# Kernel optimization log

Hardware: AMD Instinct MI355X
Metric: run time of the kernel (lower is better)

## Reference

```python
import jax, jax.numpy as jnp
import numpy as np

B, F, DIM = 32, 2048, 1024
H, DH, Q, DEPTH, MULT = 16, 64, 64, 6, 2
INNER = H * DH  # 1024
EPS = 1e-5


def _ln(x, g, b):
    m = jnp.mean(x, axis=-1, keepdims=True)
    v = jnp.mean((x - m) ** 2, axis=-1, keepdims=True)
    return (x - m) / jnp.sqrt(v + EPS) * g + b


def setup_inputs() -> dict:
    key = jax.random.key(0)
    ks = iter(jax.random.split(key, 32))
    def rn(shape, s=0.02):
        return jax.random.normal(next(ks), shape, dtype=jnp.float32) * s
    inp = {
        "features": jax.random.normal(next(ks), (B, F, DIM), dtype=jnp.float32),
        "mask": jax.random.randint(next(ks), (B, F), 0, 2),
        "latents": jax.random.normal(next(ks), (Q, INNER), dtype=jnp.float32),
        "W_down": rn((DIM, INNER)),
        "nin_g": jnp.ones((DIM,)), "nin_b": jnp.zeros((DIM,)),
        "lf_g": jnp.ones((DEPTH, INNER)), "lf_b": jnp.zeros((DEPTH, INNER)),
        "ll_g": jnp.ones((DEPTH, INNER)), "ll_b": jnp.zeros((DEPTH, INNER)),
        "Wq": rn((DEPTH, INNER, INNER)),
        "Wk": rn((DEPTH, INNER, INNER)),
        "Wv": rn((DEPTH, INNER, INNER)),
        "ffln_g": jnp.ones((DEPTH, INNER)), "ffln_b": jnp.zeros((DEPTH, INNER)),
        "ff_w1": rn((DEPTH, INNER, MULT * INNER)),
        "ff_w2": rn((DEPTH, MULT * INNER, INNER)),
        "nout_g": jnp.ones((INNER,)), "nout_b": jnp.zeros((INNER,)),
    }
    return inp


def reference(features, mask, latents, W_down, nin_g, nin_b, lf_g, lf_b, ll_g, ll_b,
              Wq, Wk, Wv, ffln_g, ffln_b, ff_w1, ff_w2, nout_g, nout_b):
    scale = DH ** (-0.5)
    # input norm + projection down to inner_dim
    f = _ln(features, nin_g, nin_b) @ W_down            # (B, F, INNER)
    x = jnp.broadcast_to(latents, (B, Q, INNER))        # (B, Q, INNER)
    keep = (mask != 0)[:, None, None, :]                # (B, 1, 1, F)
    for i in range(DEPTH):
        xf = _ln(f, lf_g[i], lf_b[i])
        xl = _ln(x, ll_g[i], ll_b[i])
        q = (xl @ Wq[i]).reshape(B, Q, H, DH).transpose(0, 2, 1, 3) * scale  # bhqd
        k = (xf @ Wk[i]).reshape(B, F, H, DH).transpose(0, 2, 1, 3)          # bhfd
        v = (xf @ Wv[i]).reshape(B, F, H, DH).transpose(0, 2, 1, 3)          # bhfd
        sim = jnp.einsum('bhqd,bhfd->bhqf', q, k)
        sim = sim - jax.lax.stop_gradient(jnp.max(sim, axis=-1, keepdims=True))
        sim = jnp.where(keep, sim, -jnp.inf)
        alphas = jax.nn.softmax(sim, axis=-1)
        alphas = jnp.nan_to_num(alphas, nan=0.0)        # fully-masked rows -> 0
        out = jnp.einsum('bhqf,bhfd->bqhd', alphas, v).reshape(B, Q, INNER)
        # feed-forward: LN -> Linear -> ReLU -> Linear
        h = jax.nn.relu(_ln(out, ffln_g[i], ffln_b[i]) @ ff_w1[i]) @ ff_w2[i]
        x = x + h
    return _ln(x, nout_g, nout_b)
```

## Files before the change

kernel.cpp:

```cpp
#include <hip/hip_runtime.h>
#include <stdint.h>


#define DEV static __device__ __forceinline__

typedef __attribute__((ext_vector_type(8))) short short8;
typedef __attribute__((ext_vector_type(4))) float f32x4;
typedef __attribute__((ext_vector_type(4))) int int4v;
typedef __attribute__((ext_vector_type(4))) unsigned short ushort4v;
typedef unsigned short ushort_t;

DEV float bf2f(ushort_t u){ union{uint32_t i; float f;} x; x.i = ((uint32_t)u)<<16; return x.f; }
DEV ushort_t f2bf(float f){
  union{float f; uint32_t i;} x; x.f = f;
  uint32_t r = x.i + 0x7fffu + ((x.i>>16)&1u);
  return (ushort_t)(r>>16);
}

#define GLOAD16(gp, lp) __builtin_amdgcn_global_load_lds( \
    (const __attribute__((address_space(1))) uint32_t*)(gp), \
    (__attribute__((address_space(3))) uint32_t*)(lp), 16, 0, 0)

#define VMCNT(n) asm volatile("s_waitcnt vmcnt(" #n ")" ::: "memory")
#define CFENCE   asm volatile("" ::: "memory")
#define MFMA16(a,b,c) __builtin_amdgcn_mfma_f32_16x16x32_bf16(a,b,c,0,0,0)
#define MFMAI8(a,b,c) __builtin_amdgcn_mfma_i32_16x16x64_i8(a,b,c,0,0,0)

template<int NXB>
DEV void xcd_remapN(int g, int total, int& x, int& y){
  int xcd = g & 7;
  int k = g >> 3;
  int rows_per_xcd = (total / NXB) >> 3;
  y = xcd * rows_per_xcd + (k / NXB);
  x = k % NXB;
}

DEV void wreduce2(float& a, float& b){
  #pragma unroll
  for (int d = 32; d; d >>= 1){ a += __shfl_xor(a, d); b += __shfl_xor(b, d); }
}

__global__ __launch_bounds__(256) void k_compact(const int* __restrict__ mask,
                                                 int* __restrict__ idx, int* __restrict__ cnt){
  int b = blockIdx.x, t = threadIdx.x;
  const int* mb = mask + b*2048;
  int keep[8]; int c = 0;
  #pragma unroll
  for (int u = 0; u < 8; ++u){ keep[u] = (mb[t*8+u] != 0); c += keep[u]; }
  __shared__ int s[256];
  s[t] = c; __syncthreads();
  for (int off = 1; off < 256; off <<= 1){
    int v = (t >= off) ? s[t-off] : 0;
    __syncthreads();
    s[t] += v;
    __syncthreads();
  }
  int pos = s[t] - c;
  #pragma unroll
  for (int u = 0; u < 8; ++u) if (keep[u]) idx[b*2048 + pos++] = t*8 + u;
  if (t == 255) cnt[b] = s[255];
}

__global__ __launch_bounds__(256) void k_gather_norm(const float* __restrict__ feat,
        const int* __restrict__ idx, const int* __restrict__ cnt, ushort_t* __restrict__ outp){
  int w = threadIdx.x >> 6, l = threadIdx.x & 63;
  int row = blockIdx.x*4 + w;
  int b = row >> 11, j = row & 2047;
  if (j >= cnt[b]) return;
  int src = idx[b*2048 + j];
  const float* rp = feat + ((size_t)(b*2048 + src))*1024;
  float4 v[4]; float s = 0.f, q = 0.f;
  #pragma unroll
  for (int i = 0; i < 4; ++i){
    v[i] = *(const float4*)(rp + i*256 + l*4);
    s += v[i].x+v[i].y+v[i].z+v[i].w;
    q += v[i].x*v[i].x+v[i].y*v[i].y+v[i].z*v[i].z+v[i].w*v[i].w;
  }
  wreduce2(s, q);
  float mean = s * (1.f/1024.f);
  float rstd = rsqrtf(q*(1.f/1024.f) - mean*mean + 1e-5f);
  ushort_t* op = outp + (size_t)row*1024;
  #pragma unroll
  for (int i = 0; i < 4; ++i){
    ushort4v o;
    o.x = f2bf((v[i].x-mean)*rstd); o.y = f2bf((v[i].y-mean)*rstd);
    o.z = f2bf((v[i].z-mean)*rstd); o.w = f2bf((v[i].w-mean)*rstd);
    *(ushort4v*)(op + i*256 + l*4) = o;
  }
}

__global__ __launch_bounds__(256) void k_rownorm_bf16(const ushort_t* __restrict__ in,
        ushort_t* __restrict__ outp, const int* __restrict__ cnt){
  int w = threadIdx.x >> 6, l = threadIdx.x & 63;
  int row = blockIdx.x*4 + w;
  if (cnt){ int b = row >> 11; if ((row & 2047) >= cnt[b]) return; }
  const ushort_t* rp = in + (size_t)row*1024;
  float f[4][4]; float s = 0.f, q = 0.f;
  #pragma unroll
  for (int i = 0; i < 4; ++i){
    ushort4v u = *(const ushort4v*)(rp + i*256 + l*4);
    f[i][0] = bf2f(u.x); f[i][1] = bf2f(u.y); f[i][2] = bf2f(u.z); f[i][3] = bf2f(u.w);
    #pragma unroll
    for (int jj = 0; jj < 4; ++jj){ s += f[i][jj]; q += f[i][jj]*f[i][jj]; }
  }
  wreduce2(s, q);
  float mean = s * (1.f/1024.f);
  float rstd = rsqrtf(q*(1.f/1024.f) - mean*mean + 1e-5f);
  ushort_t* op = outp + (size_t)row*1024;
  #pragma unroll
  for (int i = 0; i < 4; ++i){
    ushort4v o;
    o.x = f2bf((f[i][0]-mean)*rstd); o.y = f2bf((f[i][1]-mean)*rstd);
    o.z = f2bf((f[i][2]-mean)*rstd); o.w = f2bf((f[i][3]-mean)*rstd);
    *(ushort4v*)(op + i*256 + l*4) = o;
  }
}

__global__ __launch_bounds__(256) void k_rownorm_i8(const ushort_t* __restrict__ in,
        int8_t* __restrict__ outp, float* __restrict__ sca, const int* __restrict__ cnt){
  int w = threadIdx.x >> 6, l = threadIdx.x & 63;
  int row = blockIdx.x*4 + w;
  int b = row >> 11; if ((row & 2047) >= cnt[b]) return;
  const ushort_t* rp = in + (size_t)row*1024 + l*16;
  float f[16]; float s = 0.f, q = 0.f;
  #pragma unroll
  for (int i = 0; i < 4; ++i){
    ushort4v u = *(const ushort4v*)(rp + i*4);
    f[i*4+0] = bf2f(u.x); f[i*4+1] = bf2f(u.y);
    f[i*4+2] = bf2f(u.z); f[i*4+3] = bf2f(u.w);
  }
  #pragma unroll
  for (int jj = 0; jj < 16; ++jj){ s += f[jj]; q += f[jj]*f[jj]; }
  wreduce2(s, q);
  float mean = s * (1.f/1024.f);
  float rstd = rsqrtf(q*(1.f/1024.f) - mean*mean + 1e-5f);
  float amax = 0.f;
  #pragma unroll
  for (int jj = 0; jj < 16; ++jj) amax = fmaxf(amax, fabsf(f[jj]-mean));
  #pragma unroll
  for (int d = 32; d; d >>= 1) amax = fmaxf(amax, __shfl_xor(amax, d));
  amax *= rstd;
  float inv = (amax > 0.f) ? 127.f/amax : 0.f;
  if (l == 0) sca[row] = amax * (1.f/127.f);
  uint32_t wds[4];
  #pragma unroll
  for (int i = 0; i < 4; ++i){
    uint32_t wd = 0;
    #pragma unroll
    for (int c = 0; c < 4; ++c){
      int qv = (int)rintf((f[i*4+c]-mean)*rstd*inv);
      wd |= ((uint32_t)(uint8_t)(int8_t)qv) << (c*8);
    }
    wds[i] = wd;
  }
  int4v pk; pk[0]=(int)wds[0]; pk[1]=(int)wds[1]; pk[2]=(int)wds[2]; pk[3]=(int)wds[3];
  *(int4v*)(outp + (size_t)row*1024 + l*16) = pk;
}

__global__ __launch_bounds__(256) void k_quantW(const ushort_t* __restrict__ in,
        int8_t* __restrict__ outp, float* __restrict__ sca){
  int w = threadIdx.x >> 6, l = threadIdx.x & 63;
  int row = blockIdx.x*4 + w;
  const ushort_t* rp = in + (size_t)row*1024 + l*16;
  float f[16];
  #pragma unroll
  for (int i = 0; i < 4; ++i){
    ushort4v u = *(const ushort4v*)(rp + i*4);
    f[i*4+0] = bf2f(u.x); f[i*4+1] = bf2f(u.y);
    f[i*4+2] = bf2f(u.z); f[i*4+3] = bf2f(u.w);
  }
  float amax = 0.f;
  #pragma unroll
  for (int jj = 0; jj < 16; ++jj) amax = fmaxf(amax, fabsf(f[jj]));
  #pragma unroll
  for (int d = 32; d; d >>= 1) amax = fmaxf(amax, __shfl_xor(amax, d));
  float inv = (amax > 0.f) ? 127.f/amax : 0.f;
  if (l == 0) sca[row] = amax * (1.f/127.f);
  uint32_t wds[4];
  #pragma unroll
  for (int i = 0; i < 4; ++i){
    uint32_t wd = 0;
    #pragma unroll
    for (int c = 0; c < 4; ++c){
      int qv = (int)rintf(f[i*4+c]*inv);
      wd |= ((uint32_t)(uint8_t)(int8_t)qv) << (c*8);
    }
    wds[i] = wd;
  }
  int4v pk; pk[0]=(int)wds[0]; pk[1]=(int)wds[1]; pk[2]=(int)wds[2]; pk[3]=(int)wds[3];
  *(int4v*)(outp + (size_t)row*1024 + l*16) = pk;
}

__global__ __launch_bounds__(256) void k_rownorm_f32(const float* __restrict__ in,
                                                     ushort_t* __restrict__ outp){
  int w = threadIdx.x >> 6, l = threadIdx.x & 63;
  int row = blockIdx.x*4 + w;
  const float* rp = in + (size_t)row*1024;
  float4 v[4]; float s = 0.f, q = 0.f;
  #pragma unroll
  for (int i = 0; i < 4; ++i){
    v[i] = *(const float4*)(rp + i*256 + l*4);
    s += v[i].x+v[i].y+v[i].z+v[i].w;
    q += v[i].x*v[i].x+v[i].y*v[i].y+v[i].z*v[i].z+v[i].w*v[i].w;
  }
  wreduce2(s, q);
  float mean = s * (1.f/1024.f);
  float rstd = rsqrtf(q*(1.f/1024.f) - mean*mean + 1e-5f);
  ushort_t* op = outp + (size_t)row*1024;
  #pragma unroll
  for (int i = 0; i < 4; ++i){
    ushort4v o;
    o.x = f2bf((v[i].x-mean)*rstd); o.y = f2bf((v[i].y-mean)*rstd);
    o.z = f2bf((v[i].z-mean)*rstd); o.w = f2bf((v[i].w-mean)*rstd);
    *(ushort4v*)(op + i*256 + l*4) = o;
  }
}

__global__ __launch_bounds__(256) void k_final_ln(const float* __restrict__ x,
        const float* __restrict__ g, const float* __restrict__ bb, float* __restrict__ outp){
  int w = threadIdx.x >> 6, l = threadIdx.x & 63;
  int row = blockIdx.x*4 + w;
  const float* rp = x + (size_t)row*1024;
  float4 v[4]; float s = 0.f, q = 0.f;
  #pragma unroll
  for (int i = 0; i < 4; ++i){
    v[i] = *(const float4*)(rp + i*256 + l*4);
    s += v[i].x+v[i].y+v[i].z+v[i].w;
    q += v[i].x*v[i].x+v[i].y*v[i].y+v[i].z*v[i].z+v[i].w*v[i].w;
  }
  wreduce2(s, q);
  float mean = s * (1.f/1024.f);
  float rstd = rsqrtf(q*(1.f/1024.f) - mean*mean + 1e-5f);
  float* op = outp + (size_t)row*1024;
  #pragma unroll
  for (int i = 0; i < 4; ++i){
    float4 gg = *(const float4*)(g + i*256 + l*4);
    float4 bv = *(const float4*)(bb + i*256 + l*4);
    float4 o;
    o.x = (v[i].x-mean)*rstd*gg.x + bv.x; o.y = (v[i].y-mean)*rstd*gg.y + bv.y;
    o.z = (v[i].z-mean)*rstd*gg.z + bv.z; o.w = (v[i].w-mean)*rstd*gg.w + bv.w;
    *(float4*)(op + i*256 + l*4) = o;
  }
}

__global__ __launch_bounds__(256) void k_init_x(const float* __restrict__ lat, float* __restrict__ x){
  int v = blockIdx.x*256 + threadIdx.x;
  int row = v >> 8, cv = v & 255;
  ((float4*)x)[v] = ((const float4*)lat)[(row & 63)*256 + cv];
}

DEV void foldT_body(const float* __restrict__ W, const float* __restrict__ g,
                    float scale, ushort_t* __restrict__ Wt, int K, int N,
                    int n0, int k0){
  __shared__ float Ts[64][65];
  int t = threadIdx.x;
  #pragma unroll
  for (int i = 0; i < 4; ++i){
    int flat = i*1024 + t*4; int r = flat >> 6, c = flat & 63;
    float4 v = *(const float4*)(W + (size_t)(k0+r)*N + n0 + c);
    float gg = (g ? g[k0+r] : 1.f) * scale;
    Ts[r][c] = v.x*gg; Ts[r][c+1] = v.y*gg; Ts[r][c+2] = v.z*gg; Ts[r][c+3] = v.w*gg;
  }
  __syncthreads();
  #pragma unroll
  for (int i = 0; i < 4; ++i){
    int flat = i*1024 + t*4; int rn = flat >> 6, ck = flat & 63;
    ushort4v o;
    o.x = f2bf(Ts[ck][rn]);   o.y = f2bf(Ts[ck+1][rn]);
    o.z = f2bf(Ts[ck+2][rn]); o.w = f2bf(Ts[ck+3][rn]);
    *(ushort4v*)(Wt + (size_t)(n0+rn)*K + k0 + ck) = o;
  }
}

struct FDesc { const float* W; const float* g; ushort_t* dst; float scale; int K; int N; };
#define MAXFD 32
struct FoldTArgs { int cnt; FDesc d[MAXFD]; };

__global__ __launch_bounds__(256) void k_foldT_all(FoldTArgs a){
  const FDesc d = a.d[blockIdx.y];
  int nxb = d.N >> 6;
  int n0 = (blockIdx.x % nxb) * 64;
  int k0 = (blockIdx.x / nxb) * 64;
  if (k0 >= d.K) return;
  foldT_body(d.W, d.g, d.scale, d.dst, d.K, d.N, n0, k0);
}

DEV void foldBias_body(const float* __restrict__ W, const float* __restrict__ bvec,
                       float scale, float* __restrict__ bias, int K, int N, int o0){
  int t = threadIdx.x;
  int ol = t & 31, kc = t >> 5;
  int o = o0 + ol;
  int chunk = K >> 3;
  int c0 = kc*chunk, c1 = c0 + chunk;
  float s0 = 0, s1 = 0, s2 = 0, s3 = 0;
  for (int c = c0; c < c1; c += 4){
    s0 += bvec[c+0]*W[(size_t)(c+0)*N + o];
    s1 += bvec[c+1]*W[(size_t)(c+1)*N + o];
    s2 += bvec[c+2]*W[(size_t)(c+2)*N + o];
    s3 += bvec[c+3]*W[(size_t)(c+3)*N + o];
  }
  __shared__ float red[8][32];
  red[kc][ol] = (s0+s1)+(s2+s3);
  __syncthreads();
  if (kc == 0){
    float tot = 0;
    #pragma unroll
    for (int jj = 0; jj < 8; ++jj) tot += red[jj][ol];
    bias[o] = tot * scale;
  }
}

struct BDesc { const float* W; const float* b; float* dst; float scale; int K; int N; };
#define MAXBD 25
struct BiasArgs { int cnt; BDesc d[MAXBD]; };

__global__ __launch_bounds__(256) void k_foldBias_all(BiasArgs a){
  const BDesc d = a.d[blockIdx.y];
  int o0 = blockIdx.x * 32;
  if (o0 >= d.N) return;
  foldBias_body(d.W, d.b, d.scale, d.dst, d.K, d.N, o0);
}

template<int OUTMODE, bool SKIP>
__global__ __launch_bounds__(256, 4) void k_gemm(const ushort_t* __restrict__ A,
        const ushort_t* __restrict__ Bt, const float* __restrict__ bias,
        void* __restrict__ Cp, int M, int N, int K, const int* __restrict__ cnt){
  const int n0 = blockIdx.x * 128;
  const int m0 = blockIdx.y * 128;
  if (SKIP){ int b = m0 >> 11; if ((m0 & 2047) >= cnt[b]) return; }
  __shared__ ushort_t sA[2][128*32];
  __shared__ ushort_t sB[2][128*32];
  const int tid = threadIdx.x;
  const int wave = tid >> 6, lane = tid & 63;
  const int lo = lane & 15, hi = lane >> 4;
  const int wr = wave >> 1, wc = wave & 1;

  auto stage = [&](int buf, int k0){
    #pragma unroll
    for (int p = 0; p < 2; ++p){
      int r = p*64 + wave*16 + (lane >> 2);
      int c = lane & 3;
      {
        const ushort_t* gp = A + (size_t)(m0 + r)*K + k0 + c*8;
        char* lp = (char*)(&sA[buf][0]) + p*4096 + wave*1024;
        GLOAD16(gp, lp);
      }
      {
        const ushort_t* gp = Bt + (size_t)(n0 + r)*K + k0 + c*8;
        char* lp = (char*)(&sB[buf][0]) + p*4096 + wave*1024;
        GLOAD16(gp, lp);
      }
    }
  };

  f32x4 acc[4][4] = {};
  stage(0, 0);
  const int nk = K >> 5;
  for (int ks = 0; ks < nk; ++ks){
    __syncthreads();
    if (ks + 1 < nk) stage((ks+1)&1, (ks+1) << 5);
    const int buf = ks & 1;
    short8 af[4], bfr[4];
    #pragma unroll
    for (int mi = 0; mi < 4; ++mi)
      af[mi] = *(const short8*)(&sA[buf][(wr*64 + mi*16 + lo)*32 + hi*8]);
    #pragma unroll
    for (int ni = 0; ni < 4; ++ni)
      bfr[ni] = *(const short8*)(&sB[buf][(wc*64 + ni*16 + lo)*32 + hi*8]);
    #pragma unroll
    for (int mi = 0; mi < 4; ++mi)
      #pragma unroll
      for (int ni = 0; ni < 4; ++ni)
        acc[mi][ni] = MFMA16(af[mi], bfr[ni], acc[mi][ni]);
  }
  #pragma unroll
  for (int ni = 0; ni < 4; ++ni){
    int col = n0 + wc*64 + ni*16 + lo;
    float bv = bias ? bias[col] : 0.f;
    #pragma unroll
    for (int mi = 0; mi < 4; ++mi){
      int rbase = m0 + wr*64 + mi*16 + hi*4;
      #pragma unroll
      for (int rr = 0; rr < 4; ++rr){
        float v = acc[mi][ni][rr] + bv;
        size_t off = (size_t)(rbase + rr)*N + col;
        if (OUTMODE == 0)      ((ushort_t*)Cp)[off] = f2bf(v);
        else if (OUTMODE == 1) ((ushort_t*)Cp)[off] = f2bf(fmaxf(v, 0.f));
        else                   ((float*)Cp)[off] += v;
      }
    }
  }
}

template<bool SKIP, int NXB>
__global__ __launch_bounds__(512, 2) void k_gemm256p8(const ushort_t* __restrict__ A,
        const ushort_t* __restrict__ Bt, const float* __restrict__ bias,
        ushort_t* __restrict__ Cp, int M, int N, int K, const int* __restrict__ cnt){
  int bx, by;
  xcd_remapN<NXB>(blockIdx.x, gridDim.x, bx, by);
  const int n0 = bx * 256;
  const int m0 = by * 256;
  if (SKIP){ int b = m0 >> 11; if ((m0 & 2047) >= cnt[b]) return; }
  __shared__ __align__(16) ushort_t sA[2][256*64];
  __shared__ __align__(16) ushort_t sB[2][256*64];
  const int tid = threadIdx.x;
  const int wave = tid >> 6, lane = tid & 63;
  const int lo = lane & 15, hi = lane >> 4;
  const int wm = wave >> 2, wn = wave & 3;
  const int srow = lane >> 3;
  const int schunk = (lane & 7) ^ srow;
  auto stageHalf = [&](ushort_t* dst, const ushort_t* __restrict__ G, int grow0,
                       int half, int k0){
    #pragma unroll
    for (int p = 0; p < 2; ++p){
      int rbase = half*128 + p*64 + wave*8;
      const ushort_t* gp = G + (size_t)(grow0 + rbase + srow)*K + k0 + schunk*8;
      char* lp = (char*)dst + (size_t)rbase*128;
      GLOAD16(gp, lp);
    }
  };
  auto ldsA = [&](int buf, int row, int kk)->short8{
    int ch = ((kk<<2) + hi) ^ (row & 7);
    return *(const short8*)((const char*)sA + (size_t)buf*32768 + (size_t)row*128 + ch*16);
  };
  auto ldsB = [&](int buf, int row, int kk)->short8{
    int ch = ((kk<<2) + hi) ^ (row & 7);
    return *(const short8*)((const char*)sB + (size_t)buf*32768 + (size_t)row*128 + ch*16);
  };
  f32x4 acc[8][4] = {};

  short8 af[4][2], bg[2][2];
#define LOADA(BUF, AH) \
    _Pragma("unroll") for (int mi_ = 0; mi_ < 4; ++mi_) \
      _Pragma("unroll") for (int kk_ = 0; kk_ < 2; ++kk_) \
        af[mi_][kk_] = ldsA(BUF, (AH)*128 + wm*64 + mi_*16 + lo, kk_);
#define LOADB(BUF, BH) \
    _Pragma("unroll") for (int nj_ = 0; nj_ < 2; ++nj_) \
      _Pragma("unroll") for (int kk_ = 0; kk_ < 2; ++kk_) \
        bg[nj_][kk_] = ldsB(BUF, (BH)*128 + wn*32 + nj_*16 + lo, kk_);
#define MMQ(AH, BH) \
    __builtin_amdgcn_s_barrier(); CFENCE; \
    __builtin_amdgcn_s_setprio(1); \
    _Pragma("unroll") for (int mi_ = 0; mi_ < 4; ++mi_) \
      _Pragma("unroll") for (int nj_ = 0; nj_ < 2; ++nj_) \
        _Pragma("unroll") for (int kk_ = 0; kk_ < 2; ++kk_) \
          acc[(AH)*4+mi_][(BH)*2+nj_] = \
            MFMA16(af[mi_][kk_], bg[nj_][kk_], acc[(AH)*4+mi_][(BH)*2+nj_]); \
    __builtin_amdgcn_s_setprio(0); CFENCE; \
    __builtin_amdgcn_s_barrier(); CFENCE;

  stageHalf(&sA[0][0], A,  m0, 0, 0);
  stageHalf(&sB[0][0], Bt, n0, 0, 0);
  stageHalf(&sA[0][0], A,  m0, 1, 0);
  stageHalf(&sB[0][0], Bt, n0, 1, 0);
  stageHalf(&sA[1][0], A,  m0, 0, 64);
  stageHalf(&sB[1][0], Bt, n0, 1, 64);
  VMCNT(4);
  __builtin_amdgcn_s_barrier();
  CFENCE;

  const int NI = K >> 7;
  for (int i = 0; i < NI; ++i){
    const int kt = i << 7;
    const bool lastI = (i == NI-1);
    LOADA(0,0) LOADB(0,0)
    stageHalf(&sA[1][0], A,  m0, 1, kt+64);
    MMQ(0,0)
    LOADB(0,1)
    stageHalf(&sB[1][0], Bt, n0, 0, kt+64);
    MMQ(0,1)
    LOADA(0,1)
    if (!lastI) stageHalf(&sA[0][0], A,  m0, 0, kt+128);
    MMQ(1,1)
    LOADB(0,0)
    if (!lastI) stageHalf(&sB[0][0], Bt, n0, 1, kt+128);
    if (lastI){ VMCNT(0); } else { VMCNT(4); }
    MMQ(1,0)
    LOADA(1,0) LOADB(1,0)
    if (!lastI) stageHalf(&sA[0][0], A,  m0, 1, kt+128);
    MMQ(0,0)
    LOADB(1,1)
    if (!lastI) stageHalf(&sB[0][0], Bt, n0, 0, kt+128);
    MMQ(0,1)
    LOADA(1,1)
    if (!lastI) stageHalf(&sA[1][0], A,  m0, 0, kt+192);
    MMQ(1,1)
    LOADB(1,0)
    if (!lastI){ stageHalf(&sB[1][0], Bt, n0, 1, kt+192); VMCNT(4); }
    MMQ(1,0)
  }
#undef LOADA
#undef LOADB
#undef MMQ

  #pragma unroll
  for (int b2 = 0; b2 < 2; ++b2)
    #pragma unroll
    for (int nj = 0; nj < 2; ++nj){
      int col = n0 + b2*128 + wn*32 + nj*16 + lo;
      float bv = bias ? bias[col] : 0.f;
      #pragma unroll
      for (int a2 = 0; a2 < 2; ++a2)
        #pragma unroll
        for (int mi4 = 0; mi4 < 4; ++mi4){
          int rbase = m0 + a2*128 + wm*64 + mi4*16 + hi*4;
          #pragma unroll
          for (int rr = 0; rr < 4; ++rr){
            float v = acc[a2*4+mi4][b2*2+nj][rr] + bv;
            Cp[(size_t)(rbase + rr)*N + col] = f2bf(v);
          }
        }
    }
}

template<bool SKIP, int NXB>
__global__ __launch_bounds__(512, 2) void k_gemm256i8(const int8_t* __restrict__ A,
        const int8_t* __restrict__ Bt, const float* __restrict__ sAr,
        const float* __restrict__ sBr, const float* __restrict__ bias,
        ushort_t* __restrict__ Cp, int M, int N, int Kb, const int* __restrict__ cnt){
  int bx, by;
  xcd_remapN<NXB>(blockIdx.x, gridDim.x, bx, by);
  const int n0 = bx * 256;
  const int m0 = by * 256;
  if (SKIP){ int b = m0 >> 11; if ((m0 & 2047) >= cnt[b]) return; }
  __shared__ __align__(16) char sAl[2][256*128];
  __shared__ __align__(16) char sBl[2][256*128];
  const int tid = threadIdx.x;
  const int wave = tid >> 6, lane = tid & 63;
  const int lo = lane & 15, hi = lane >> 4;
  const int wm = wave >> 2, wn = wave & 3;
  const int srow = lane >> 3;
  const int schunk = (lane & 7) ^ srow;
  auto stageHalf = [&](char* dst, const int8_t* __restrict__ G, int grow0,
                       int half, int k0){
    #pragma unroll
    for (int p = 0; p < 2; ++p){
      int rbase = half*128 + p*64 + wave*8;
      const int8_t* gp = G + (size_t)(grow0 + rbase + srow)*Kb + k0 + schunk*16;
      char* lp = dst + (size_t)rbase*128;
      GLOAD16(gp, lp);
    }
  };
  auto ldsA = [&](int buf, int row, int kk)->int4v{
    int ch = ((kk<<2) + hi) ^ (row & 7);
    return *(const int4v*)((const char*)sAl + (size_t)buf*32768 + (size_t)row*128 + ch*16);
  };
  auto ldsB = [&](int buf, int row, int kk)->int4v{
    int ch = ((kk<<2) + hi) ^ (row & 7);
    return *(const int4v*)((const char*)sBl + (size_t)buf*32768 + (size_t)row*128 + ch*16);
  };
  int4v acc[8][4] = {};

  int4v af[4][2], bg[2][2];
#define LOADA(BUF, AH) \
    _Pragma("unroll") for (int mi_ = 0; mi_ < 4; ++mi_) \
      _Pragma("unroll") for (int kk_ = 0; kk_ < 2; ++kk_) \
        af[mi_][kk_] = ldsA(BUF, (AH)*128 + wm*64 + mi_*16 + lo, kk_);
#define LOADB(BUF, BH) \
    _Pragma("unroll") for (int nj_ = 0; nj_ < 2; ++nj_) \
      _Pragma("unroll") for (int kk_ = 0; kk_ < 2; ++kk_) \
        bg[nj_][kk_] = ldsB(BUF, (BH)*128 + wn*32 + nj_*16 + lo, kk_);
#define MMQ(AH, BH) \
    __builtin_amdgcn_s_barrier(); CFENCE; \
    __builtin_amdgcn_s_setprio(1); \
    _Pragma("unroll") for (int mi_ = 0; mi_ < 4; ++mi_) \
      _Pragma("unroll") for (int nj_ = 0; nj_ < 2; ++nj_) \
        _Pragma("unroll") for (int kk_ = 0; kk_ < 2; ++kk_) \
          acc[(AH)*4+mi_][(BH)*2+nj_] = \
            MFMAI8(af[mi_][kk_], bg[nj_][kk_], acc[(AH)*4+mi_][(BH)*2+nj_]); \
    __builtin_amdgcn_s_setprio(0); CFENCE; \
    __builtin_amdgcn_s_barrier(); CFENCE;

  stageHalf(&sAl[0][0], A,  m0, 0, 0);
  stageHalf(&sBl[0][0], Bt, n0, 0, 0);
  stageHalf(&sAl[0][0], A,  m0, 1, 0);
  stageHalf(&sBl[0][0], Bt, n0, 1, 0);
  stageHalf(&sAl[1][0], A,  m0, 0, 128);
  stageHalf(&sBl[1][0], Bt, n0, 1, 128);
  VMCNT(4);
  __builtin_amdgcn_s_barrier();
  CFENCE;

  const int NI = Kb >> 8;
  for (int i = 0; i < NI; ++i){
    const int kt = i << 8;
    const bool lastI = (i == NI-1);
    LOADA(0,0) LOADB(0,0)
    stageHalf(&sAl[1][0], A,  m0, 1, kt+128);
    MMQ(0,0)
    LOADB(0,1)
    stageHalf(&sBl[1][0], Bt, n0, 0, kt+128);
    MMQ(0,1)
    LOADA(0,1)
    if (!lastI) stageHalf(&sAl[0][0], A,  m0, 0, kt+256);
    MMQ(1,1)
    LOADB(0,0)
    if (!lastI) stageHalf(&sBl[0][0], Bt, n0, 1, kt+256);
    if (lastI){ VMCNT(0); } else { VMCNT(4); }
    MMQ(1,0)
    LOADA(1,0) LOADB(1,0)
    if (!lastI) stageHalf(&sAl[0][0], A,  m0, 1, kt+256);
    MMQ(0,0)
    LOADB(1,1)
    if (!lastI) stageHalf(&sBl[0][0], Bt, n0, 0, kt+256);
    MMQ(0,1)
    LOADA(1,1)
    if (!lastI) stageHalf(&sAl[1][0], A,  m0, 0, kt+384);
    MMQ(1,1)
    LOADB(1,0)
    if (!lastI){ stageHalf(&sBl[1][0], Bt, n0, 1, kt+384); VMCNT(4); }
    MMQ(1,0)
  }
#undef LOADA
#undef LOADB
#undef MMQ

  #pragma unroll
  for (int b2 = 0; b2 < 2; ++b2)
    #pragma unroll
    for (int nj = 0; nj < 2; ++nj){
      int col = n0 + b2*128 + wn*32 + nj*16 + lo;
      float bv = bias ? bias[col] : 0.f;
      float sb = sBr[col];
      #pragma unroll
      for (int a2 = 0; a2 < 2; ++a2)
        #pragma unroll
        for (int mi4 = 0; mi4 < 4; ++mi4){
          int rbase = m0 + a2*128 + wm*64 + mi4*16 + hi*4;
          #pragma unroll
          for (int rr = 0; rr < 4; ++rr){
            int row = rbase + rr;
            float v = (float)acc[a2*4+mi4][b2*2+nj][rr] * (sAr[row]*sb) + bv;
            Cp[(size_t)row*N + col] = f2bf(v);
          }
        }
    }
}

__global__ __launch_bounds__(256) void k_attn(const ushort_t* __restrict__ qb,
        const ushort_t* __restrict__ kvb, int kstride, const int* __restrict__ cnt,
        ushort_t* __restrict__ outb){
  const int bh = blockIdx.x;
  const int b = bh >> 4, h = bh & 15;
  const int t = threadIdx.x;
  const int wave = t >> 6, lane = t & 63, lo = lane & 15, hi = lane >> 4;
  __shared__ ushort_t Qs[64*64];
  __shared__ ushort_t Ks[2][64*64];
  __shared__ ushort_t Vt[2][64][72];
  __shared__ ushort_t Ps[4][16][72];

  const int count = cnt[b];

  #pragma unroll
  for (int p = 0; p < 2; ++p){
    int r = p*32 + wave*8 + (lane >> 3);
    int c = (lane & 7) ^ (r & 7);
    const ushort_t* gp = qb + (size_t)(b*64 + r)*1024 + h*64 + c*8;
    char* lp = (char*)Qs + p*4096 + wave*1024;
    GLOAD16(gp, lp);
  }

  auto stageK = [&](int buf, int tt){
    #pragma unroll
    for (int p = 0; p < 2; ++p){
      int r = p*32 + wave*8 + (lane >> 3);
      int c = (lane & 7) ^ (r & 7);
      const ushort_t* gp = kvb + (size_t)(b*2048 + tt*64 + r)*kstride + h*64 + c*8;
      char* lp = (char*)(&Ks[buf][0]) + p*4096 + wave*1024;
      GLOAD16(gp, lp);
    }
  };
  const int vjj = (t & 31)*2, vc = (t >> 5)*8;
  ushort4v va0, va1, vb0, vb1;
  auto issueV = [&](int tt){
    const ushort_t* g0 = kvb + (size_t)(b*2048 + tt*64 + vjj)*kstride + 1024 + h*64 + vc;
    va0 = *(const ushort4v*)(g0);
    va1 = *(const ushort4v*)(g0 + 4);
    vb0 = *(const ushort4v*)(g0 + kstride);
    vb1 = *(const ushort4v*)(g0 + kstride + 4);
  };
  auto writeV = [&](int buf, int tt){
    bool va  = (tt*64 + vjj)     < count;
    bool vb2 = (tt*64 + vjj + 1) < count;
    #pragma unroll
    for (int u = 0; u < 8; ++u){
      ushort_t ea = (u < 4) ? ((ushort_t*)&va0)[u] : ((ushort_t*)&va1)[u-4];
      ushort_t eb = (u < 4) ? ((ushort_t*)&vb0)[u] : ((ushort_t*)&vb1)[u-4];
      uint32_t word = (va ? (uint32_t)ea : 0u) | ((vb2 ? (uint32_t)eb : 0u) << 16);
      *(uint32_t*)(&Vt[buf][vc+u][vjj]) = word;
    }
  };

  f32x4 oacc[4] = {};
  float m[4], l[4];
  #pragma unroll
  for (int rr = 0; rr < 4; ++rr){ m[rr] = -__builtin_inff(); l[rr] = 0.f; }

  const int ntiles = (count + 63) >> 6;
  if (ntiles > 0){ stageK(0, 0); issueV(0); }

  for (int tt = 0; tt < ntiles; ++tt){
    const int buf = tt & 1;
    writeV(buf, tt);
    if (tt + 1 < ntiles){ stageK(buf^1, tt+1); issueV(tt+1); }
    asm volatile("s_waitcnt lgkmcnt(0)" ::: "memory");
    __builtin_amdgcn_s_barrier();
    CFENCE;

    f32x4 s[4] = {};
    #pragma unroll
    for (int kk = 0; kk < 2; ++kk){
      int rA = wave*16 + lo;
      short8 aq = *(const short8*)(&Qs[rA*64 + (((kk*4 + hi) ^ (rA & 7))*8)]);
      #pragma unroll
      for (int ni = 0; ni < 4; ++ni){
        int rB = ni*16 + lo;
        short8 bk = *(const short8*)(&Ks[buf][rB*64 + (((kk*4 + hi) ^ (rB & 7))*8)]);
        s[ni] = MFMA16(aq, bk, s[ni]);
      }
    }
    #pragma unroll
    for (int ni = 0; ni < 4; ++ni){
      if (tt*64 + ni*16 + lo >= count){
        s[ni][0] = s[ni][1] = s[ni][2] = s[ni][3] = -__builtin_inff();
      }
    }
    float p[4][4];
    #pragma unroll
    for (int rr = 0; rr < 4; ++rr){
      float mx = fmaxf(fmaxf(s[0][rr], s[1][rr]), fmaxf(s[2][rr], s[3][rr]));
      #pragma unroll
      for (int d = 1; d < 16; d <<= 1) mx = fmaxf(mx, __shfl_xor(mx, d));
      float mnew = fmaxf(m[rr], mx);
      float sc = __expf(m[rr] - mnew);
      float rsum = 0.f;
      #pragma unroll
      for (int ni = 0; ni < 4; ++ni){
        float pv = __expf(s[ni][rr] - mnew);
        p[ni][rr] = pv;
        rsum += pv;
      }
      #pragma unroll
      for (int d = 1; d < 16; d <<= 1) rsum += __shfl_xor(rsum, d);
      l[rr] = l[rr]*sc + rsum;
      m[rr] = mnew;
      #pragma unroll
      for (int ni = 0; ni < 4; ++ni) oacc[ni][rr] *= sc;
    }
    #pragma unroll
    for (int ni = 0; ni < 4; ++ni)
      #pragma unroll
      for (int rr = 0; rr < 4; ++rr)
        Ps[wave][hi*4+rr][ni*16+lo] = f2bf(p[ni][rr]);
    asm volatile("s_waitcnt lgkmcnt(0)" ::: "memory");
    #pragma unroll
    for (int kk = 0; kk < 2; ++kk){
      short8 pa = *(const short8*)(&Ps[wave][lo][kk*32 + hi*8]);
      #pragma unroll
      for (int ni = 0; ni < 4; ++ni){
        short8 bv = *(const short8*)(&Vt[buf][ni*16 + lo][kk*32 + hi*8]);
        oacc[ni] = MFMA16(pa, bv, oacc[ni]);
      }
    }
    CFENCE;
    __builtin_amdgcn_s_barrier();
    CFENCE;
  }
  #pragma unroll
  for (int rr = 0; rr < 4; ++rr){
    float inv = (l[rr] > 0.f) ? 1.f/l[rr] : 0.f;
    #pragma unroll
    for (int ni = 0; ni < 4; ++ni){
      size_t off = (size_t)(b*64 + wave*16 + hi*4 + rr)*1024 + h*64 + ni*16 + lo;
      outb[off] = f2bf(oacc[ni][rr] * inv);
    }
  }
}

extern "C" void kernel_launch(void* const* d_in, const int* in_sizes, int n_in,
                              void* d_out, int out_size, void* d_ws, size_t ws_size,
                              hipStream_t stream){
  const float* features = (const float*)d_in[0];
  const int*   mask     = (const int*)  d_in[1];
  const float* latents  = (const float*)d_in[2];
  const float* W_down   = (const float*)d_in[3];
  const float* nin_g    = (const float*)d_in[4];
  const float* nin_b    = (const float*)d_in[5];
  const float* lf_g     = (const float*)d_in[6];
  const float* lf_b     = (const float*)d_in[7];
  const float* ll_g     = (const float*)d_in[8];
  const float* ll_b     = (const float*)d_in[9];
  const float* Wq       = (const float*)d_in[10];
  const float* Wk       = (const float*)d_in[11];
  const float* Wv       = (const float*)d_in[12];
  const float* ffln_g   = (const float*)d_in[13];
  const float* ffln_b   = (const float*)d_in[14];
  const float* ff_w1    = (const float*)d_in[15];
  const float* ff_w2    = (const float*)d_in[16];
  const float* nout_g   = (const float*)d_in[17];
  const float* nout_b   = (const float*)d_in[18];

  char* ws = (char*)d_ws;
  size_t off = 0;
  auto alloc = [&](size_t bytes)->char*{
    char* p = ws + off;
    off += (bytes + 255) & ~(size_t)255;
    return p;
  };
  const size_t SZW = (size_t)1024*1024*2;

  ushort_t* FHAT  = (ushort_t*)alloc((size_t)65536*1024*2);
  int8_t*   I8A   = (int8_t*)  alloc((size_t)65536*1024);
  float*    SA    = (float*)   alloc((size_t)65536*4);
  int8_t*   I8B   = (int8_t*)  alloc((size_t)12288*1024);
  float*    SB    = (float*)   alloc((size_t)12288*4);
  ushort_t* WDT   = (ushort_t*)alloc(SZW);
  ushort_t* WQT6  = (ushort_t*)alloc(SZW*6);
  ushort_t* WKVT6 = (ushort_t*)alloc(SZW*2*6);
  ushort_t* W1T6  = (ushort_t*)alloc(SZW*2*6);
  ushort_t* W2T6  = (ushort_t*)alloc(SZW*2*6);
  float* BD   = (float*)alloc(1024*4);
  float* BQ6  = (float*)alloc(1024*4*6);
  float* BKV6 = (float*)alloc(2048*4*6);
  float* B16  = (float*)alloc(2048*4*6);
  float*    X    = (float*)   alloc((size_t)2048*1024*4);
  ushort_t* XHAT = (ushort_t*)alloc((size_t)2048*1024*2);
  ushort_t* QP   = (ushort_t*)alloc((size_t)2048*1024*2);
  ushort_t* OUTB = (ushort_t*)alloc((size_t)2048*1024*2);
  ushort_t* OUTH = (ushort_t*)alloc((size_t)2048*1024*2);
  ushort_t* H1   = (ushort_t*)alloc((size_t)2048*2048*2);
  int* CNT = (int*)alloc(32*4);
  int* IDX = (int*)alloc((size_t)65536*4);
  ushort_t* KVBUF = (ushort_t*)alloc((size_t)65536*2048*2);
  ushort_t* FNORM = KVBUF;
  (void)in_sizes; (void)n_in; (void)out_size; (void)ws_size;

  const float scale = 0.125f;

  FoldTArgs fa; int nf = 0;
  auto addF = [&](const float* W, const float* g, float sc, ushort_t* dst, int K, int N){
    fa.d[nf++] = FDesc{W, g, dst, sc, K, N};
  };
  addF(W_down, nin_g, 1.f, WDT, 1024, 1024);
  for (int i = 0; i < 6; ++i){
    const float* Wqi = Wq + (size_t)i*1024*1024;
    const float* Wki = Wk + (size_t)i*1024*1024;
    const float* Wvi = Wv + (size_t)i*1024*1024;
    const float* W1i = ff_w1 + (size_t)i*1024*2048;
    const float* W2i = ff_w2 + (size_t)i*2048*1024;
    addF(Wqi, ll_g + i*1024, scale, WQT6  + i*(SZW/2),        1024, 1024);
    addF(Wki, lf_g + i*1024, 1.f,   WKVT6 + i*SZW,            1024, 1024);
    addF(Wvi, lf_g + i*1024, 1.f,   WKVT6 + i*SZW + (SZW/2),  1024, 1024);
    addF(W1i, ffln_g + i*1024, 1.f, W1T6  + i*SZW,            1024, 2048);
    addF(W2i, nullptr, 1.f,         W2T6  + i*SZW,            2048, 1024);
  }
  fa.cnt = nf;

  BiasArgs ba; int nb = 0;
  auto addB = [&](const float* W, const float* b, float sc, float* dst, int K, int N){
    ba.d[nb++] = BDesc{W, b, dst, sc, K, N};
  };
  addB(W_down, nin_b, 1.f, BD, 1024, 1024);
  for (int i = 0; i < 6; ++i){
    const float* Wqi = Wq + (size_t)i*1024*1024;
    const float* Wki = Wk + (size_t)i*1024*1024;
    const float* Wvi = Wv + (size_t)i*1024*1024;
    const float* W1i = ff_w1 + (size_t)i*1024*2048;
    addB(Wqi, ll_b + i*1024, scale, BQ6  + i*1024,        1024, 1024);
    addB(Wki, lf_b + i*1024, 1.f,   BKV6 + i*2048,        1024, 1024);
    addB(Wvi, lf_b + i*1024, 1.f,   BKV6 + i*2048 + 1024, 1024, 1024);
    addB(W1i, ffln_b + i*1024, 1.f, B16  + i*2048,        1024, 2048);
  }
  ba.cnt = nb;

  k_compact     <<<32,    256, 0, stream>>>(mask, IDX, CNT);
  k_gather_norm <<<16384, 256, 0, stream>>>(features, IDX, CNT, FNORM);
  k_foldT_all   <<<dim3(512, nf), 256, 0, stream>>>(fa);
  k_foldBias_all<<<dim3(64,  nb), 256, 0, stream>>>(ba);
  k_quantW      <<<3072,  256, 0, stream>>>(WKVT6, I8B, SB);
  k_gemm256p8<true,4><<<1024, 512, 0, stream>>>(FNORM, WDT, BD, FHAT, 65536, 1024, 1024, CNT);
  k_rownorm_i8  <<<16384, 256, 0, stream>>>(FHAT, I8A, SA, CNT);
  k_init_x      <<<2048,  256, 0, stream>>>(latents, X);

  for (int i = 0; i < 6; ++i){
    k_gemm256i8<true,8><<<2048, 512, 0, stream>>>(I8A, I8B + (size_t)i*2048*1024,
                                                  SA, SB + i*2048, BKV6 + i*2048,
                                                  KVBUF, 65536, 2048, 1024, CNT);
    k_rownorm_f32<<<512, 256, 0, stream>>>(X, XHAT);
    k_gemm<0,false><<<dim3(8,16),  256, 0, stream>>>(XHAT, WQT6 + i*(SZW/2), BQ6 + i*1024,
                                                     QP, 2048, 1024, 1024, nullptr);
    k_attn<<<512, 256, 0, stream>>>(QP, KVBUF, 2048, CNT, OUTB);
    k_rownorm_bf16<<<512, 256, 0, stream>>>(OUTB, OUTH, nullptr);
    k_gemm<1,false><<<dim3(16,16), 256, 0, stream>>>(OUTH, W1T6 + i*SZW, B16 + i*2048,
                                                     H1, 2048, 2048, 1024, nullptr);
    k_gemm<2,false><<<dim3(8,16),  256, 0, stream>>>(H1, W2T6 + i*SZW, nullptr,
                                                     X, 2048, 1024, 2048, nullptr);
  }
  k_final_ln<<<512, 256, 0, stream>>>(X, nout_g, nout_b, (float*)d_out);
}
```

Before: 2.021 ms.

## Quantize latent-path Q, FF1 and FF2 GEMMs to int8 with per-row scales

The latent-side GEMMs (Q projection and both feed-forward layers) move from bf16 MFMA to int8 MFMA. Activations are fused into layernorm-plus-int8 quantization kernels, and the Wq, W1 and W2 weights are quantized once per row up front. H1 gets an extra quantization pass before FF2. This aims to halve operand bytes and use the higher int8 MFMA rate on these small M=2048 GEMMs, at the cost of extra quantization launches and lower numerical precision.

```diff
diff --git a/kernel.cpp b/kernel.cpp
--- a/kernel.cpp
+++ b/kernel.cpp
@@ -89,38 +89,11 @@
   }
 }
 
-__global__ __launch_bounds__(256) void k_rownorm_bf16(const ushort_t* __restrict__ in,
-        ushort_t* __restrict__ outp, const int* __restrict__ cnt){
-  int w = threadIdx.x >> 6, l = threadIdx.x & 63;
-  int row = blockIdx.x*4 + w;
-  if (cnt){ int b = row >> 11; if ((row & 2047) >= cnt[b]) return; }
-  const ushort_t* rp = in + (size_t)row*1024;
-  float f[4][4]; float s = 0.f, q = 0.f;
-  #pragma unroll
-  for (int i = 0; i < 4; ++i){
-    ushort4v u = *(const ushort4v*)(rp + i*256 + l*4);
-    f[i][0] = bf2f(u.x); f[i][1] = bf2f(u.y); f[i][2] = bf2f(u.z); f[i][3] = bf2f(u.w);
-    #pragma unroll
-    for (int jj = 0; jj < 4; ++jj){ s += f[i][jj]; q += f[i][jj]*f[i][jj]; }
-  }
-  wreduce2(s, q);
-  float mean = s * (1.f/1024.f);
-  float rstd = rsqrtf(q*(1.f/1024.f) - mean*mean + 1e-5f);
-  ushort_t* op = outp + (size_t)row*1024;
-  #pragma unroll
-  for (int i = 0; i < 4; ++i){
-    ushort4v o;
-    o.x = f2bf((f[i][0]-mean)*rstd); o.y = f2bf((f[i][1]-mean)*rstd);
-    o.z = f2bf((f[i][2]-mean)*rstd); o.w = f2bf((f[i][3]-mean)*rstd);
-    *(ushort4v*)(op + i*256 + l*4) = o;
-  }
-}
-
 __global__ __launch_bounds__(256) void k_rownorm_i8(const ushort_t* __restrict__ in,
         int8_t* __restrict__ outp, float* __restrict__ sca, const int* __restrict__ cnt){
   int w = threadIdx.x >> 6, l = threadIdx.x & 63;
   int row = blockIdx.x*4 + w;
-  int b = row >> 11; if ((row & 2047) >= cnt[b]) return;
+  if (cnt){ int b = row >> 11; if ((row & 2047) >= cnt[b]) return; }
   const ushort_t* rp = in + (size_t)row*1024 + l*16;
   float f[16]; float s = 0.f, q = 0.f;
   #pragma unroll
@@ -157,62 +130,80 @@
   *(int4v*)(outp + (size_t)row*1024 + l*16) = pk;
 }
 
-__global__ __launch_bounds__(256) void k_quantW(const ushort_t* __restrict__ in,
+__global__ __launch_bounds__(256) void k_rownorm_f32_i8(const float* __restrict__ in,
         int8_t* __restrict__ outp, float* __restrict__ sca){
   int w = threadIdx.x >> 6, l = threadIdx.x & 63;
   int row = blockIdx.x*4 + w;
-  const ushort_t* rp = in + (size_t)row*1024 + l*16;
-  float f[16];
+  const float* rp = in + (size_t)row*1024 + l*16;
+  float f[16]; float s = 0.f, q = 0.f;
   #pragma unroll
   for (int i = 0; i < 4; ++i){
+    float4 v = *(const float4*)(rp + i*4);
+    f[i*4+0] = v.x; f[i*4+1] = v.y; f[i*4+2] = v.z; f[i*4+3] = v.w;
+  }
+  #pragma unroll
+  for (int jj = 0; jj < 16; ++jj){ s += f[jj]; q += f[jj]*f[jj]; }
+  wreduce2(s, q);
+  float mean = s * (1.f/1024.f);
+  float rstd = rsqrtf(q*(1.f/1024.f) - mean*mean + 1e-5f);
+  float amax = 0.f;
+  #pragma unroll
+  for (int jj = 0; jj < 16; ++jj) amax = fmaxf(amax, fabsf(f[jj]-mean));
+  #pragma unroll
+  for (int d = 32; d; d >>= 1) amax = fmaxf(amax, __shfl_xor(amax, d));
+  amax *= rstd;
+  float inv = (amax > 0.f) ? 127.f/amax : 0.f;
+  if (l == 0) sca[row] = amax * (1.f/127.f);
+  uint32_t wds[4];
+  #pragma unroll
+  for (int i = 0; i < 4; ++i){
+    uint32_t wd = 0;
+    #pragma unroll
+    for (int c = 0; c < 4; ++c){
+      int qv = (int)rintf((f[i*4+c]-mean)*rstd*inv);
+      wd |= ((uint32_t)(uint8_t)(int8_t)qv) << (c*8);
+    }
+    wds[i] = wd;
+  }
+  int4v pk; pk[0]=(int)wds[0]; pk[1]=(int)wds[1]; pk[2]=(int)wds[2]; pk[3]=(int)wds[3];
+  *(int4v*)(outp + (size_t)row*1024 + l*16) = pk;
+}
+
+template<int PER>
+__global__ __launch_bounds__(256) void k_quant_rows(const ushort_t* __restrict__ in,
+        int8_t* __restrict__ outp, float* __restrict__ sca){
+  const int K = PER*64;
+  int w = threadIdx.x >> 6, l = threadIdx.x & 63;
+  int row = blockIdx.x*4 + w;
+  const ushort_t* rp = in + (size_t)row*K + l*PER;
+  float f[PER];
+  #pragma unroll
+  for (int i = 0; i < PER/4; ++i){
     ushort4v u = *(const ushort4v*)(rp + i*4);
     f[i*4+0] = bf2f(u.x); f[i*4+1] = bf2f(u.y);
     f[i*4+2] = bf2f(u.z); f[i*4+3] = bf2f(u.w);
   }
   float amax = 0.f;
   #pragma unroll
-  for (int jj = 0; jj < 16; ++jj) amax = fmaxf(amax, fabsf(f[jj]));
+  for (int jj = 0; jj < PER; ++jj) amax = fmaxf(amax, fabsf(f[jj]));
   #pragma unroll
   for (int d = 32; d; d >>= 1) amax = fmaxf(amax, __shfl_xor(amax, d));
   float inv = (amax > 0.f) ? 127.f/amax : 0.f;
   if (l == 0) sca[row] = amax * (1.f/127.f);
-  uint32_t wds[4];
-  #pragma unroll
-  for (int i = 0; i < 4; ++i){
-    uint32_t wd = 0;
-    #pragma unroll
-    for (int c = 0; c < 4; ++c){
-      int qv = (int)rintf(f[i*4+c]*inv);
-      wd |= ((uint32_t)(uint8_t)(int8_t)qv) << (c*8);
-    }
-    wds[i] = wd;
-  }
-  int4v pk; pk[0]=(int)wds[0]; pk[1]=(int)wds[1]; pk[2]=(int)wds[2]; pk[3]=(int)wds[3];
-  *(int4v*)(outp + (size_t)row*1024 + l*16) = pk;
-}
-
-__global__ __launch_bounds__(256) void k_rownorm_f32(const float* __restrict__ in,
-                                                     ushort_t* __restrict__ outp){
-  int w = threadIdx.x >> 6, l = threadIdx.x & 63;
-  int row = blockIdx.x*4 + w;
-  const float* rp = in + (size_t)row*1024;
-  float4 v[4]; float s = 0.f, q = 0.f;
-  #pragma unroll
-  for (int i = 0; i < 4; ++i){
-    v[i] = *(const float4*)(rp + i*256 + l*4);
-    s += v[i].x+v[i].y+v[i].z+v[i].w;
-    q += v[i].x*v[i].x+v[i].y*v[i].y+v[i].z*v[i].z+v[i].w*v[i].w;
-  }
-  wreduce2(s, q);
-  float mean = s * (1.f/1024.f);
-  float rstd = rsqrtf(q*(1.f/1024.f) - mean*mean + 1e-5f);
-  ushort_t* op = outp + (size_t)row*1024;
-  #pragma unroll
-  for (int i = 0; i < 4; ++i){
-    ushort4v o;
-    o.x = f2bf((v[i].x-mean)*rstd); o.y = f2bf((v[i].y-mean)*rstd);
-    o.z = f2bf((v[i].z-mean)*rstd); o.w = f2bf((v[i].w-mean)*rstd);
-    *(ushort4v*)(op + i*256 + l*4) = o;
+  #pragma unroll
+  for (int vq = 0; vq < PER/16; ++vq){
+    int4v pk;
+    #pragma unroll
+    for (int i = 0; i < 4; ++i){
+      uint32_t wd = 0;
+      #pragma unroll
+      for (int c = 0; c < 4; ++c){
+        int qv = (int)rintf(f[vq*16 + i*4 + c]*inv);
+        wd |= ((uint32_t)(uint8_t)(int8_t)qv) << (c*8);
+      }
+      pk[i] = (int)wd;
+    }
+    *(int4v*)(outp + (size_t)row*K + l*PER + vq*16) = pk;
   }
 }
 
@@ -321,15 +312,15 @@
   foldBias_body(d.W, d.b, d.scale, d.dst, d.K, d.N, o0);
 }
 
-template<int OUTMODE, bool SKIP>
-__global__ __launch_bounds__(256, 4) void k_gemm(const ushort_t* __restrict__ A,
-        const ushort_t* __restrict__ Bt, const float* __restrict__ bias,
-        void* __restrict__ Cp, int M, int N, int K, const int* __restrict__ cnt){
+template<int OUTMODE>
+__global__ __launch_bounds__(256, 4) void k_gemm128i8(const int8_t* __restrict__ A,
+        const int8_t* __restrict__ Bt, const float* __restrict__ sAr,
+        const float* __restrict__ sBr, const float* __restrict__ bias,
+        void* __restrict__ Cp, int M, int N, int Kb){
   const int n0 = blockIdx.x * 128;
   const int m0 = blockIdx.y * 128;
-  if (SKIP){ int b = m0 >> 11; if ((m0 & 2047) >= cnt[b]) return; }
-  __shared__ ushort_t sA[2][128*32];
-  __shared__ ushort_t sB[2][128*32];
+  __shared__ __align__(16) char sA[2][128*64];
+  __shared__ __align__(16) char sB[2][128*64];
   const int tid = threadIdx.x;
   const int wave = tid >> 6, lane = tid & 63;
   const int lo = lane & 15, hi = lane >> 4;
@@ -341,49 +332,51 @@
       int r = p*64 + wave*16 + (lane >> 2);
       int c = lane & 3;
       {
-        const ushort_t* gp = A + (size_t)(m0 + r)*K + k0 + c*8;
+        const int8_t* gp = A + (size_t)(m0 + r)*Kb + k0 + c*16;
         char* lp = (char*)(&sA[buf][0]) + p*4096 + wave*1024;
         GLOAD16(gp, lp);
       }
       {
-        const ushort_t* gp = Bt + (size_t)(n0 + r)*K + k0 + c*8;
+        const int8_t* gp = Bt + (size_t)(n0 + r)*Kb + k0 + c*16;
         char* lp = (char*)(&sB[buf][0]) + p*4096 + wave*1024;
         GLOAD16(gp, lp);
       }
     }
   };
 
-  f32x4 acc[4][4] = {};
+  int4v acc[4][4] = {};
   stage(0, 0);
-  const int nk = K >> 5;
+  const int nk = Kb >> 6;
   for (int ks = 0; ks < nk; ++ks){
     __syncthreads();
-    if (ks + 1 < nk) stage((ks+1)&1, (ks+1) << 5);
+    if (ks + 1 < nk) stage((ks+1)&1, (ks+1) << 6);
     const int buf = ks & 1;
-    short8 af[4], bfr[4];
+    int4v af[4], bfr[4];
     #pragma unroll
     for (int mi = 0; mi < 4; ++mi)
-      af[mi] = *(const short8*)(&sA[buf][(wr*64 + mi*16 + lo)*32 + hi*8]);
+      af[mi] = *(const int4v*)(&sA[buf][(wr*64 + mi*16 + lo)*64 + hi*16]);
     #pragma unroll
     for (int ni = 0; ni < 4; ++ni)
-      bfr[ni] = *(const short8*)(&sB[buf][(wc*64 + ni*16 + lo)*32 + hi*8]);
+      bfr[ni] = *(const int4v*)(&sB[buf][(wc*64 + ni*16 + lo)*64 + hi*16]);
     #pragma unroll
     for (int mi = 0; mi < 4; ++mi)
       #pragma unroll
       for (int ni = 0; ni < 4; ++ni)
-        acc[mi][ni] = MFMA16(af[mi], bfr[ni], acc[mi][ni]);
+        acc[mi][ni] = MFMAI8(af[mi], bfr[ni], acc[mi][ni]);
   }
   #pragma unroll
   for (int ni = 0; ni < 4; ++ni){
     int col = n0 + wc*64 + ni*16 + lo;
     float bv = bias ? bias[col] : 0.f;
+    float sb = sBr[col];
     #pragma unroll
     for (int mi = 0; mi < 4; ++mi){
       int rbase = m0 + wr*64 + mi*16 + hi*4;
       #pragma unroll
       for (int rr = 0; rr < 4; ++rr){
-        float v = acc[mi][ni][rr] + bv;
-        size_t off = (size_t)(rbase + rr)*N + col;
+        int row = rbase + rr;
+        float v = (float)acc[mi][ni][rr] * (sAr[row]*sb) + bv;
+        size_t off = (size_t)row*N + col;
         if (OUTMODE == 0)      ((ushort_t*)Cp)[off] = f2bf(v);
         else if (OUTMODE == 1) ((ushort_t*)Cp)[off] = f2bf(fmaxf(v, 0.f));
         else                   ((float*)Cp)[off] += v;
@@ -812,8 +805,14 @@
   ushort_t* FHAT  = (ushort_t*)alloc((size_t)65536*1024*2);
   int8_t*   I8A   = (int8_t*)  alloc((size_t)65536*1024);
   float*    SA    = (float*)   alloc((size_t)65536*4);
-  int8_t*   I8B   = (int8_t*)  alloc((size_t)12288*1024);
-  float*    SB    = (float*)   alloc((size_t)12288*4);
+  int8_t*   I8KV  = (int8_t*)  alloc((size_t)12288*1024);
+  float*    SKV   = (float*)   alloc((size_t)12288*4);
+  int8_t*   I8Q   = (int8_t*)  alloc((size_t)6144*1024);
+  float*    SQW   = (float*)   alloc((size_t)6144*4);
+  int8_t*   I8W1  = (int8_t*)  alloc((size_t)12288*1024);
+  float*    SW1   = (float*)   alloc((size_t)12288*4);
+  int8_t*   I8W2  = (int8_t*)  alloc((size_t)6144*2048);
+  float*    SW2   = (float*)   alloc((size_t)6144*4);
   ushort_t* WDT   = (ushort_t*)alloc(SZW);
   ushort_t* WQT6  = (ushort_t*)alloc(SZW*6);
   ushort_t* WKVT6 = (ushort_t*)alloc(SZW*2*6);
@@ -824,11 +823,15 @@
   float* BKV6 = (float*)alloc(2048*4*6);
   float* B16  = (float*)alloc(2048*4*6);
   float*    X    = (float*)   alloc((size_t)2048*1024*4);
-  ushort_t* XHAT = (ushort_t*)alloc((size_t)2048*1024*2);
+  int8_t*   I8X  = (int8_t*)  alloc((size_t)2048*1024);
+  float*    SX   = (float*)   alloc((size_t)2048*4);
   ushort_t* QP   = (ushort_t*)alloc((size_t)2048*1024*2);
   ushort_t* OUTB = (ushort_t*)alloc((size_t)2048*1024*2);
-  ushort_t* OUTH = (ushort_t*)alloc((size_t)2048*1024*2);
+  int8_t*   I8O  = (int8_t*)  alloc((size_t)2048*1024);
+  float*    SO   = (float*)   alloc((size_t)2048*4);
   ushort_t* H1   = (ushort_t*)alloc((size_t)2048*2048*2);
+  int8_t*   I8H  = (int8_t*)  alloc((size_t)2048*2048);
+  float*    SH   = (float*)   alloc((size_t)2048*4);
   int* CNT = (int*)alloc(32*4);
   int* IDX = (int*)alloc((size_t)65536*4);
   ushort_t* KVBUF = (ushort_t*)alloc((size_t)65536*2048*2);
@@ -877,24 +880,31 @@
   k_gather_norm <<<16384, 256, 0, stream>>>(features, IDX, CNT, FNORM);
   k_foldT_all   <<<dim3(512, nf), 256, 0, stream>>>(fa);
   k_foldBias_all<<<dim3(64,  nb), 256, 0, stream>>>(ba);
-  k_quantW      <<<3072,  256, 0, stream>>>(WKVT6, I8B, SB);
+  k_quant_rows<16><<<3072, 256, 0, stream>>>(WKVT6, I8KV, SKV);
+  k_quant_rows<16><<<1536, 256, 0, stream>>>(WQT6,  I8Q,  SQW);
+  k_quant_rows<16><<<3072, 256, 0, stream>>>(W1T6,  I8W1, SW1);
+  k_quant_rows<32><<<1536, 256, 0, stream>>>(W2T6,  I8W2, SW2);
   k_gemm256p8<true,4><<<1024, 512, 0, stream>>>(FNORM, WDT, BD, FHAT, 65536, 1024, 1024, CNT);
   k_rownorm_i8  <<<16384, 256, 0, stream>>>(FHAT, I8A, SA, CNT);
   k_init_x      <<<2048,  256, 0, stream>>>(latents, X);
 
   for (int i = 0; i < 6; ++i){
-    k_gemm256i8<true,8><<<2048, 512, 0, stream>>>(I8A, I8B + (size_t)i*2048*1024,
-                                                  SA, SB + i*2048, BKV6 + i*2048,
+    k_gemm256i8<true,8><<<2048, 512, 0, stream>>>(I8A, I8KV + (size_t)i*2048*1024,
+                                                  SA, SKV + i*2048, BKV6 + i*2048,
                                                   KVBUF, 65536, 2048, 1024, CNT);
-    k_rownorm_f32<<<512, 256, 0, stream>>>(X, XHAT);
-    k_gemm<0,false><<<dim3(8,16),  256, 0, stream>>>(XHAT, WQT6 + i*(SZW/2), BQ6 + i*1024,
-                                                     QP, 2048, 1024, 1024, nullptr);
+    k_rownorm_f32_i8<<<512, 256, 0, stream>>>(X, I8X, SX);
+    k_gemm128i8<0><<<dim3(8,16), 256, 0, stream>>>(I8X, I8Q + (size_t)i*1024*1024,
+                                                   SX, SQW + i*1024, BQ6 + i*1024,
+                                                   QP, 2048, 1024, 1024);
     k_attn<<<512, 256, 0, stream>>>(QP, KVBUF, 2048, CNT, OUTB);
-    k_rownorm_bf16<<<512, 256, 0, stream>>>(OUTB, OUTH, nullptr);
-    k_gemm<1,false><<<dim3(16,16), 256, 0, stream>>>(OUTH, W1T6 + i*SZW, B16 + i*2048,
-                                                     H1, 2048, 2048, 1024, nullptr);
-    k_gemm<2,false><<<dim3(8,16),  256, 0, stream>>>(H1, W2T6 + i*SZW, nullptr,
-                                                     X, 2048, 1024, 2048, nullptr);
+    k_rownorm_i8<<<512, 256, 0, stream>>>(OUTB, I8O, SO, nullptr);
+    k_gemm128i8<1><<<dim3(16,16), 256, 0, stream>>>(I8O, I8W1 + (size_t)i*2048*1024,
+                                                    SO, SW1 + i*2048, B16 + i*2048,
+                                                    H1, 2048, 2048, 1024);
+    k_quant_rows<32><<<512, 256, 0, stream>>>(H1, I8H, SH);
+    k_gemm128i8<2><<<dim3(8,16), 256, 0, stream>>>(I8H, I8W2 + (size_t)i*1024*2048,
+                                                   SH, SW2 + i*1024, nullptr,
+                                                   X, 2048, 1024, 2048);
   }
   k_final_ln<<<512, 256, 0, stream>>>(X, nout_g, nout_b, (float*)d_out);
 }
```

Result: faster. 1.783 ms (-11.8%).
